# Optimization experiments

Hardware: AMD Instinct MI355X
Metric: run time of the kernel (lower is better)

## Reference

```python
import jax, jax.numpy as jnp
import numpy as np

V, E, H = 32000, 256, 512   # vocab, embed_dim, hidden_dim
B, S, T = 16, 512, 128      # batch, src_len, tgt_len
PAD = 0
H2 = 2 * H                  # decoder hidden size


def setup_inputs() -> dict:
    key = jax.random.key(0)
    ks = jax.random.split(key, 20)
    g = lambda k, shape: jax.random.normal(k, shape, dtype=jnp.float32) * 0.05
    emb = g(ks[0], (V, E)).at[PAD].set(0.0)  # padding_idx row zeroed
    inp = {
        "src": jax.random.randint(ks[18], (B, S), 0, V, dtype=jnp.int32),
        "tgt": jax.random.randint(ks[19], (B, T), 0, V, dtype=jnp.int32),
        "emb": emb,
        # encoder forward direction (torch gate order i,f,g,o)
        "Wih_f": g(ks[1], (4 * H, E)), "Whh_f": g(ks[2], (4 * H, H)),
        "bih_f": g(ks[3], (4 * H,)),   "bhh_f": g(ks[4], (4 * H,)),
        # encoder backward direction
        "Wih_b": g(ks[5], (4 * H, E)), "Whh_b": g(ks[6], (4 * H, H)),
        "bih_b": g(ks[7], (4 * H,)),   "bhh_b": g(ks[8], (4 * H,)),
        # decoder LSTM: input E+2H, hidden 2H
        "Wih_d": g(ks[9], (4 * H2, E + H2)), "Whh_d": g(ks[10], (4 * H2, H2)),
        "bih_d": g(ks[11], (4 * H2,)),       "bhh_d": g(ks[12], (4 * H2,)),
        # attention Linear(4H -> 2H)
        "Wa": g(ks[13], (H2, 2 * H2)), "ba": g(ks[14], (H2,)),
        # output Linear(2H -> V)
        "Wo": g(ks[15], (V, H2)), "bo": g(ks[16], (V,)),
    }
    return inp


def _lstm_cell(x, h, c, Wih, Whh, bih, bhh):
    z = x @ Wih.T + h @ Whh.T + bih + bhh
    i, f, g, o = jnp.split(z, 4, axis=-1)
    c = jax.nn.sigmoid(f) * c + jax.nn.sigmoid(i) * jnp.tanh(g)
    h = jax.nn.sigmoid(o) * jnp.tanh(c)
    return h, c


def _lstm_scan(xs, h0, c0, Wih, Whh, bih, bhh):
    def step(carry, x):
        h, c = _lstm_cell(x, carry[0], carry[1], Wih, Whh, bih, bhh)
        return (h, c), h
    (hT, cT), hs = jax.lax.scan(step, (h0, c0), xs)
    return hs, hT, cT


def reference(src, tgt, emb, Wih_f, Whh_f, bih_f, bhh_f, Wih_b, Whh_b, bih_b, bhh_b,
              Wih_d, Whh_d, bih_d, bhh_d, Wa, ba, Wo, bo):
    z = jnp.zeros((B, H), dtype=emb.dtype)
    xs = emb[src].transpose(1, 0, 2)                       # [S,B,E]
    hs_f, hTf, _ = _lstm_scan(xs,        z, z, Wih_f, Whh_f, bih_f, bhh_f)
    hs_b, hTb, _ = _lstm_scan(xs[::-1],  z, z, Wih_b, Whh_b, bih_b, bhh_b)
    enc_out = jnp.concatenate([hs_f, hs_b[::-1]], -1).transpose(1, 0, 2)  # [B,S,2H]
    h = jnp.concatenate([hTf, hTb], -1)                    # decoder h0 [B,2H]
    c = jnp.zeros_like(h)  # note: original reuses encoder c_n; see combined c0 below
    # original uses c_n (last cells) as decoder c0:
    _, _, cTf = _lstm_scan(xs, z, z, Wih_f, Whh_f, bih_f, bhh_f)[1], None, None
    # recompute cleanly (scan already returned cT above; redo properly):
    hs_f2, hTf2, cTf2 = _lstm_scan(xs,       z, z, Wih_f, Whh_f, bih_f, bhh_f)
    hs_b2, hTb2, cTb2 = _lstm_scan(xs[::-1], z, z, Wih_b, Whh_b, bih_b, bhh_b)
    c = jnp.concatenate([cTf2, cTb2], -1)

    Wa_h, Wa_e = Wa[:, :H2], Wa[:, H2:]
    enc_proj = jnp.einsum('bsd,kd->bsk', enc_out, Wa_e) + ba  # [B,S,2H]

    dec_xs = emb[tgt[:, :T - 1]].transpose(1, 0, 2)        # [T-1,B,E] teacher-forced

    def dec_step(carry, x):
        h, c = carry
        energy = jnp.tanh(enc_proj + (h @ Wa_h.T)[:, None, :])  # [B,S,2H]
        w = jax.nn.softmax(energy.sum(-1), axis=1)              # [B,S]
        ctx = jnp.einsum('bs,bsd->bd', w, enc_out)              # [B,2H]
        xi = jnp.concatenate([x, ctx], -1)                      # [B,E+2H]
        h, c = _lstm_cell(xi, h, c, Wih_d, Whh_d, bih_d, bhh_d)
        pred = h @ Wo.T + bo                                    # [B,V]
        return (h, c), pred

    _, preds = jax.lax.scan(dec_step, (h, c), dec_xs)           # [T-1,B,V]
    outputs = jnp.concatenate(
        [jnp.zeros((B, 1, V), dtype=preds.dtype), preds.transpose(1, 0, 2)], axis=1)
    return outputs
```

## Files before the change

### kernel.cpp

```cpp
#include <hip/hip_runtime.h>

typedef unsigned int uint;
typedef unsigned short ushort;
typedef unsigned long long ull;
typedef __attribute__((ext_vector_type(8))) short bf16x8;
typedef __attribute__((ext_vector_type(4))) float f32x4;

static constexpr int V_ = 32000, E_ = 256, H_ = 512, B_ = 16, S_ = 512, T_ = 128;
static constexpr int H2_ = 1024, G4_ = 2048, D4_ = 4096, KXI_ = 2304;
static constexpr int DSTEPS = T_ - 1;
static constexpr int MD = 2048;
static constexpr int NWG_DEC = 256;
static constexpr float LOG2E = 1.4426950408889634f;
static constexpr int ASTR = 2312;

#define DEVFN __device__ __forceinline__

DEVFN ushort f2bf(float f){ uint u = __builtin_bit_cast(uint, f); u += 0x7fffu + ((u>>16)&1u); return (ushort)(u>>16); }
DEVFN float bf2f(ushort h){ uint u = ((uint)h)<<16; return __builtin_bit_cast(float, u); }
DEVFN float fsig(float x){ float e = __builtin_amdgcn_exp2f(-LOG2E*x); return __builtin_amdgcn_rcpf(1.f+e); }
DEVFN float ftanh(float x){ x = fminf(15.f,fmaxf(-15.f,x)); float e = __builtin_amdgcn_exp2f(2.f*LOG2E*x); return (e-1.f)*__builtin_amdgcn_rcpf(e+1.f); }
DEVFN f32x4 mfma16(bf16x8 a, bf16x8 b, f32x4 c){ return __builtin_amdgcn_mfma_f32_16x16x32_bf16(a,b,c,0,0,0); }

struct ull2v{ ull x, y; };
DEVFN ull ald64(const void* p){ return __hip_atomic_load((const ull*)p, __ATOMIC_RELAXED, __HIP_MEMORY_SCOPE_AGENT); }
DEVFN uint ald32u(const uint* p){ return __hip_atomic_load(p, __ATOMIC_RELAXED, __HIP_MEMORY_SCOPE_AGENT); }
DEVFN float ald_f32(const float* p){ uint v = __hip_atomic_load((const uint*)p, __ATOMIC_RELAXED, __HIP_MEMORY_SCOPE_AGENT); return __builtin_bit_cast(float, v); }
DEVFN void ast32(float* p, float v){ __hip_atomic_store(p, v, __ATOMIC_RELAXED, __HIP_MEMORY_SCOPE_AGENT); }
DEVFN void ast16(ushort* p, ushort v){ __hip_atomic_store(p, v, __ATOMIC_RELAXED, __HIP_MEMORY_SCOPE_AGENT); }
DEVFN void astu(uint* p, uint v){ __hip_atomic_store(p, v, __ATOMIC_RELAXED, __HIP_MEMORY_SCOPE_AGENT); }

DEVFN void lbar(uint* lflags, int grp, int mem, int tid, uint& rnd){
  __syncthreads();
  rnd++;
  if (tid==0) astu(lflags + grp*16 + mem, rnd);
  if (tid<16){
    while (ald32u(lflags + grp*16 + tid) < rnd) __builtin_amdgcn_s_sleep(1);
  }
  __syncthreads();
}

__global__ void k_init(uint* __restrict__ flags, uint* __restrict__ hgf, uint* __restrict__ hgb,
                       uint* __restrict__ hU, uint* __restrict__ ctxU){
  int i = blockIdx.x*256 + threadIdx.x;
  if (i < 1024) flags[i] = 0;
  if (i < 2*B_*H_){ hgf[i]=0u; hgb[i]=0u; }
  if (i < B_*H2_) hU[i] = 0u;
  if (i < 2*B_*H2_) ctxU[i] = 0u;
}

__global__ void k_embed(const int* __restrict__ src, const int* __restrict__ tgt,
                        const float* __restrict__ emb, ushort* __restrict__ Xb, ushort* __restrict__ DXb){
  int r = blockIdx.x, tid = threadIdx.x;
  if (r < S_*B_){
    int s = r>>4, b = r&15;
    int id = src[b*S_+s];
    Xb[(size_t)r*E_+tid] = f2bf(emb[(size_t)id*E_+tid]);
  } else {
    int r2 = r - S_*B_;
    int t = r2>>4, b = r2&15;
    int id = tgt[b*T_+t];
    DXb[(size_t)r2*E_+tid] = f2bf(emb[(size_t)id*E_+tid]);
  }
}

__global__ void k_cvt_encw(const float* __restrict__ src, ushort* __restrict__ dst){
  int d = blockIdx.x;
  int wg = d>>7, r = d&127;
  int w = r>>4, jj=(r>>2)&3, g=r&3;
  int srow = g*H_ + wg*32 + w*4 + jj;
  for (int c = threadIdx.x; c < E_; c += 256)
    dst[(size_t)d*E_ + c] = f2bf(src[(size_t)srow*E_ + c]);
}

__global__ void k_bias_encp(const float* __restrict__ bih, const float* __restrict__ bhh, float* __restrict__ dst){
  int d = blockIdx.x*256 + threadIdx.x;
  int wg = d>>7, r = d&127;
  int w = r>>4, jj=(r>>2)&3, g=r&3;
  int srow = g*H_ + wg*32 + w*4 + jj;
  dst[d] = bih[srow]+bhh[srow];
}

__global__ void k_cvt_decw(const float* __restrict__ Wih_d, const float* __restrict__ Whh_d,
                           ushort* __restrict__ dst){
  int d = blockIdx.x;
  int wg = d>>4, r = d&15, jj = r>>2, g = r&3;
  int srow = g*H2_ + wg*4 + jj;
  for (int c = threadIdx.x; c < KXI_; c += 256){
    float v = (c < E_+H2_) ? Wih_d[(size_t)srow*(E_+H2_) + c] : Whh_d[(size_t)srow*H2_ + (c - (E_+H2_))];
    dst[(size_t)d*KXI_ + c] = f2bf(v);
  }
}

__global__ void k_bias_decp(const float* __restrict__ bih, const float* __restrict__ bhh, float* __restrict__ dst){
  int d = blockIdx.x*256 + threadIdx.x;
  int wg = d>>4, r = d&15, jj = r>>2, g = r&3;
  int srow = g*H2_ + wg*4 + jj;
  dst[d] = bih[srow]+bhh[srow];
}

__global__ void k_cvt_strided(const float* __restrict__ src, ushort* __restrict__ dst,
                              int cols, int sld, int soff, int dld, int doff){
  int r = blockIdx.x;
  for (int c = threadIdx.x; c < cols; c += 256)
    dst[(size_t)r*dld + doff + c] = f2bf(src[(size_t)r*sld + soff + c]);
}

__global__ void k_zero_t0(float* __restrict__ out){
  int i = blockIdx.x*256 + threadIdx.x;
  if (i < B_*V_){ int b = i / V_, v = i - b*V_; out[(size_t)b*T_*V_ + v] = 0.f; }
}

template<int MODE>
__global__ __launch_bounds__(256) void gemm128(const ushort* __restrict__ A, const ushort* __restrict__ Bm,
    const float* __restrict__ bias, void* __restrict__ outp, int M, int N, int K, int Mvalid){
  __shared__ __align__(16) ushort As[128*32];
  __shared__ __align__(16) ushort Bs[128*32];
  int tid = threadIdx.x;
  int wave = tid>>6, lane = tid&63;
  int m0 = blockIdx.y*128, n0 = blockIdx.x*128;
  int wm = wave>>1, wn = wave&1;
  int col = lane&15, rg = lane>>4;
  f32x4 acc[4][4];
  #pragma unroll
  for (int i=0;i<4;i++)
    #pragma unroll
    for (int j=0;j<4;j++) acc[i][j] = {0.f,0.f,0.f,0.f};
  for (int k0=0;k0<K;k0+=32){
    __syncthreads();
    #pragma unroll
    for (int j=0;j<2;j++){
      int li = j*256+tid;
      int row = li>>2, ko = (li&3)*8;
      *(bf16x8*)(As + li*8) = *(const bf16x8*)(A + (size_t)(m0+row)*K + k0 + ko);
      *(bf16x8*)(Bs + li*8) = *(const bf16x8*)(Bm + (size_t)(n0+row)*K + k0 + ko);
    }
    __syncthreads();
    bf16x8 af[4], bfr[4];
    #pragma unroll
    for (int f=0;f<4;f++){
      af[f]  = *(const bf16x8*)(As + (wm*64+f*16+col)*32 + rg*8);
      bfr[f] = *(const bf16x8*)(Bs + (wn*64+f*16+col)*32 + rg*8);
    }
    #pragma unroll
    for (int fm=0;fm<4;fm++)
      #pragma unroll
      for (int fn=0;fn<4;fn++)
        acc[fm][fn] = mfma16(af[fm], bfr[fn], acc[fm][fn]);
  }
  #pragma unroll
  for (int fm=0;fm<4;fm++){
    int mrow = m0 + wm*64 + fm*16 + rg*4;
    #pragma unroll
    for (int fn=0;fn<4;fn++){
      int gcol = n0 + wn*64 + fn*16 + col;
      float bv = bias ? bias[gcol] : 0.f;
      #pragma unroll
      for (int i=0;i<4;i++){
        float v = acc[fm][fn][i] + bv;
        int grow = mrow + i;
        if (MODE==0) ((float*)outp)[(size_t)grow*N + gcol] = v;
        else if (MODE==1) ((ushort*)outp)[(size_t)grow*N + gcol] = f2bf(v);
        else if (MODE==3) ((ushort*)outp)[(size_t)(grow>>4)*(16*2048) + gcol*16 + (grow&15)] = f2bf(v);
        else { if (grow < Mvalid){ int b = grow&15, t = grow>>4;
               ((float*)outp)[(size_t)b*T_*V_ + (size_t)(t+1)*V_ + gcol] = v; } }
      }
    }
  }
}

__global__ __launch_bounds__(512) void k_enc_persist(
    const ushort* __restrict__ Xgf, const ushort* __restrict__ Xgb,
    const float* __restrict__ Whhf, const float* __restrict__ Whhb,
    ushort* __restrict__ enc, ushort* __restrict__ enct,
    uint* __restrict__ hbuf1, float* __restrict__ cbuf0,
    uint* __restrict__ hgf, uint* __restrict__ hgb){
  const int dir = blockIdx.x >> 4;
  const int wg  = blockIdx.x & 15;
  const ushort* Xg = dir ? Xgb : Xgf;
  const float* Whh = dir ? Whhb : Whhf;
  uint* hg = dir ? hgb : hgf;
  __shared__ __align__(16) ushort Wlds[128*512];
  __shared__ __align__(16) ushort hls[16*512];
  int tid = threadIdx.x;
  for (int it=0; it<32; ++it){
    int r = it*4 + (tid>>7), ct = tid&127;
    int w_ = r>>4, jj=(r>>2)&3, g=r&3;
    int srow = g*H_ + wg*32 + w_*4 + jj;
    float4 v = *(const float4*)(Whh + (size_t)srow*H_ + ct*4);
    ushort4 o; o.x=f2bf(v.x); o.y=f2bf(v.y); o.z=f2bf(v.z); o.w=f2bf(v.w);
    int byte = (r*1024 + ct*8) ^ ((r&7)<<4);
    *(ushort4*)((char*)Wlds + byte) = o;
  }
  int w = tid>>6, lane = tid&63, colL = lane&15, rg = lane>>4;
  int gg = colL&3;
  float cst[4];
  #pragma unroll
  for (int i=0;i<4;i++) cst[i]=0.f;
  __syncthreads();
  for (int t=0;t<S_;++t){
    int pos = dir ? (S_-1-t) : t;
    const uint* hsrcU = hg + (t&1)*B_*H_;
    int colg = wg*128 + w*16 + colL;
    ushort4 xv = *(const ushort4*)(Xg + ((size_t)pos*2048 + colg)*16 + rg*4);
    uint uu[16];
    for(;;){
      #pragma unroll
      for (int k2=0;k2<2;k2++){
        int idx = tid + k2*512;
        const uint* p = hsrcU + (idx>>6)*H_ + (idx&63)*8;
        #pragma unroll
        for (int j=0;j<4;j++){
          ull v = ald64(p + j*2);
          uu[k2*8+j*2] = (uint)v; uu[k2*8+j*2+1] = (uint)(v>>32);
        }
      }
      bool ok = true;
      #pragma unroll
      for (int i2=0;i2<16;i2++) ok &= ((uu[i2]>>16) == (uint)t);
      if (ok) break;
      __builtin_amdgcn_s_sleep(1);
    }
    f32x4 acc;
    acc[0]=bf2f(xv.x); acc[1]=bf2f(xv.y); acc[2]=bf2f(xv.z); acc[3]=bf2f(xv.w);
    #pragma unroll
    for (int k2=0;k2<2;k2++){
      int idx = tid + k2*512;
      int byte = ((idx>>6)*1024 + (idx&63)*16) ^ (((idx>>6)&7)<<4);
      ushort tmp[8];
      #pragma unroll
      for (int j=0;j<8;j++) tmp[j] = (ushort)uu[k2*8+j];
      *(bf16x8*)((char*)hls + byte) = *(bf16x8*)tmp;
    }
    __syncthreads();
    int rowb = w*16 + colL;
    int base = rowb*1024 + rg*16, xm = (rowb&7)<<4;
    int hbase = colL*1024 + rg*16, hxm = (colL&7)<<4;
    #pragma unroll
    for (int kt=0;kt<16;kt++){
      bf16x8 afv = *(const bf16x8*)((const char*)hls + ((hbase + kt*64) ^ hxm));
      bf16x8 bfv = *(const bf16x8*)((const char*)Wlds + ((base + kt*64) ^ xm));
      acc = mfma16(afv, bfv, acc);
    }
    uint* hdstU = hg + ((t+1)&1)*B_*H_;
    #pragma unroll
    for (int i=0;i<4;i++){
      float v0 = acc[i];
      float v1 = __shfl_xor(v0, 1);
      float v2 = __shfl_xor(v0, 2);
      float v3 = __shfl_xor(v1, 2);
      float zi = gg==0?v0: gg==1?v1: gg==2?v2: v3;
      float zf = (gg^1)==0?v0: (gg^1)==1?v1: (gg^1)==2?v2: v3;
      float zg = (gg^2)==0?v0: (gg^2)==1?v1: (gg^2)==2?v2: v3;
      float zo = (gg^3)==0?v0: (gg^3)==1?v1: (gg^3)==2?v2: v3;
      float cc = fsig(zf)*cst[i] + fsig(zi)*ftanh(zg);
      cst[i] = cc;
      float h = fsig(zo)*ftanh(cc);
      if (gg==0){
        int j = wg*32 + w*4 + (colL>>2);
        int b = rg*4+i;
        ushort hb = f2bf(h);
        enc[((size_t)b*S_ + pos)*H2_ + dir*H_ + j] = hb;
        enct[((size_t)b*H2_ + dir*H_ + j)*S_ + pos] = hb;
        astu(&hdstU[b*H_ + j], (uint)hb | ((uint)(t+1)<<16));
        if (t==S_-1){
          hbuf1[b*H2_ + dir*H_ + j] = (uint)hb;
          cbuf0[b*H2_ + dir*H_ + j] = cc;
        }
      }
    }
    __syncthreads();
  }
}

__global__ __launch_bounds__(512) void k_dec(
    const float* __restrict__ P, const ushort* __restrict__ WaH,
    const ushort* __restrict__ Wd, const float* __restrict__ bsd,
    const ushort* __restrict__ enct, const ushort* __restrict__ DXb,
    const float* __restrict__ cbuf0, uint* __restrict__ hU,
    uint* __restrict__ ctxU, float* __restrict__ qbuf,
    float* __restrict__ scores, ushort* __restrict__ hsd,
    uint* __restrict__ flags){
  __shared__ __align__(16) ushort AB[16*ASTR];
  __shared__ __align__(16) float pr[8*256];
  __shared__ float redz[256];
  __shared__ float qls[1024];
  __shared__ float wls[512];
  __shared__ float part[512];
  __shared__ float red[16];
  __shared__ float cst[64];
  uint* lflags = flags + 256;
  uint* qf     = flags + 768;
  int wgid = blockIdx.x, tid = threadIdx.x;
  int w = tid>>6, lane = tid&63, colL = lane&15, rg = lane>>4;
  int b = wgid>>4, wc = wgid&15;
  uint rnd = 0;
  if (tid < 64){
    int jj = tid>>4, b4 = tid&15;
    cst[tid] = cbuf0[b4*H2_ + wgid*4 + jj];
  }
  for (int st=0; st<DSTEPS; ++st){
    const uint* hprevU = hU + ((st+1)&1)*B_*H2_;
    uint* cslot = ctxU + (st&1)*B_*H2_;
    const uint wantH = (uint)st;
    const uint wantC = (uint)(st+1);
    float* qslot = qbuf + (st&1)*B_*H2_;
    if (wgid >= 64 && wgid < 128){
      int n0 = (wgid-64)*16;
      const ushort* Bp = WaH + (size_t)(n0+colL)*H2_ + w*128 + rg*8;
      bf16x8 bwa[4];
      #pragma unroll
      for (int kt=0;kt<4;kt++) bwa[kt] = *(const bf16x8*)(Bp + kt*32);
      const uint* hp = hprevU + colL*H2_ + w*128 + rg*8;
      uint uu[32];
      for(;;){
        #pragma unroll
        for (int kt=0;kt<4;kt++)
          #pragma unroll
          for (int j=0;j<4;j++){
            ull v = ald64(hp + kt*32 + j*2);
            uu[kt*8+j*2] = (uint)v; uu[kt*8+j*2+1] = (uint)(v>>32);
          }
        bool ok = true;
        #pragma unroll
        for (int i2=0;i2<32;i2++) ok &= ((uu[i2]>>16) == wantH);
        if (ok) break;
        __builtin_amdgcn_s_sleep(1);
      }
      f32x4 acc = {0.f,0.f,0.f,0.f};
      #pragma unroll
      for (int kt=0;kt<4;kt++){
        ushort tmp[8];
        #pragma unroll
        for (int j=0;j<8;j++) tmp[j] = (ushort)uu[kt*8+j];
        acc = mfma16(*(bf16x8*)tmp, bwa[kt], acc);
      }
      *(f32x4*)&pr[w*256 + lane*4] = acc;
      __syncthreads();
      if (tid < 256){
        float s = pr[tid];
        #pragma unroll
        for (int w8=1;w8<8;w8++) s += pr[w8*256 + tid];
        int l = tid>>2, i = tid&3;
        ast32(&qslot[(size_t)((l>>4)*4 + i)*H2_ + n0 + (l&15)], s);
      }
      __syncthreads();
      if (tid==0) astu(qf + (wgid-64), wantC);
    }
    f32x4 pv[16];
    {
      int rbase = b*S_ + wc*32 + w*4;
      #pragma unroll
      for (int rr=0;rr<4;rr++){
        const f32x4* Pr = (const f32x4*)(P + (size_t)(rbase+rr)*H2_) + lane*4;
        #pragma unroll
        for (int u=0;u<4;u++) pv[rr*4+u] = Pr[u];
      }
    }
    if (tid < 64){
      while (ald32u(qf + tid) < wantC) __builtin_amdgcn_s_sleep(1);
    }
    __syncthreads();
    {
      ull q2 = ald64((const ull*)(qslot + (size_t)b*H2_) + tid);
      *(ull*)&qls[tid*2] = q2;
      __syncthreads();
      f32x4 qv[4];
      #pragma unroll
      for (int u=0;u<4;u++) qv[u] = *(const f32x4*)&qls[lane*16 + u*4];
      int rbase = b*S_ + wc*32 + w*4;
      #pragma unroll
      for (int rr=0;rr<4;rr++){
        float s = 0.f;
        #pragma unroll
        for (int u=0;u<4;u++){
          f32x4 p4 = pv[rr*4+u];
          s += ftanh(p4[0]+qv[u][0])+ftanh(p4[1]+qv[u][1])+ftanh(p4[2]+qv[u][2])+ftanh(p4[3]+qv[u][3]);
        }
        #pragma unroll
        for (int o=32;o;o>>=1) s += __shfl_xor(s,o);
        if (lane==0) ast32(&scores[rbase+rr], s);
      }
    }
    bf16x8 ev[8];
    {
      int c = wc*64 + (tid&63), sseg = tid>>6;
      const ushort* ep = enct + ((size_t)b*H2_ + c)*S_ + sseg*64;
      #pragma unroll
      for (int u=0;u<8;u++) ev[u] = *(const bf16x8*)(ep + u*8);
    }
    lbar(lflags, b, wc, tid, rnd);
    {
      float sc = ald_f32(scores + b*S_ + tid);
      float m = sc;
      #pragma unroll
      for (int o=32;o;o>>=1) m = fmaxf(m, __shfl_xor(m,o));
      if (lane==0) red[w] = m;
      __syncthreads();
      m = red[0];
      #pragma unroll
      for (int k2=1;k2<8;k2++) m = fmaxf(m, red[k2]);
      float e = __builtin_amdgcn_exp2f((sc - m)*LOG2E);
      float ss = e;
      #pragma unroll
      for (int o=32;o;o>>=1) ss += __shfl_xor(ss,o);
      if (lane==0) red[8+w] = ss;
      __syncthreads();
      float tot = red[8];
      #pragma unroll
      for (int k2=9;k2<16;k2++) tot += red[k2];
      wls[tid] = e * __builtin_amdgcn_rcpf(tot);
      __syncthreads();
      int sseg = tid>>6;
      float a = 0.f;
      #pragma unroll
      for (int u=0;u<8;u++){
        #pragma unroll
        for (int j=0;j<8;j++) a += wls[sseg*64 + u*8 + j] * bf2f((ushort)ev[u][j]);
      }
      part[tid] = a;
      __syncthreads();
      if (tid < 64){
        float s = part[tid];
        #pragma unroll
        for (int g2=1;g2<8;g2++) s += part[g2*64 + tid];
        astu(&cslot[b*H2_ + wc*64 + tid], (uint)f2bf(s) | (wantC<<16));
      }
    }
    {
      { int b3 = tid>>5, seg = tid&31;
        *(bf16x8*)&AB[b3*ASTR + seg*8] = *(const bf16x8*)(DXb + (size_t)(st*16+b3)*E_ + seg*8); }
      bf16x8 bw[9];
      {
        int row0 = wgid*16;
        const ushort* Bp = Wd + (size_t)(row0+colL)*KXI_ + w*288 + rg*8;
        #pragma unroll
        for (int kt=0;kt<9;kt++) bw[kt] = *(const bf16x8*)(Bp + kt*32);
      }
      uint uc[32], uh[32];
      for(;;){
        #pragma unroll
        for (int k2=0;k2<4;k2++){
          int idx = tid + k2*512;
          const uint* pc = cslot  + (idx>>7)*H2_ + (idx&127)*8;
          const uint* ph = hprevU + (idx>>7)*H2_ + (idx&127)*8;
          #pragma unroll
          for (int j=0;j<4;j++){
            ull vc = ald64(pc + j*2);
            ull vh = ald64(ph + j*2);
            uc[k2*8+j*2] = (uint)vc; uc[k2*8+j*2+1] = (uint)(vc>>32);
            uh[k2*8+j*2] = (uint)vh; uh[k2*8+j*2+1] = (uint)(vh>>32);
          }
        }
        bool ok = true;
        #pragma unroll
        for (int i2=0;i2<32;i2++) ok &= ((uc[i2]>>16) == wantC) && ((uh[i2]>>16) == wantH);
        if (ok) break;
        __builtin_amdgcn_s_sleep(1);
      }
      #pragma unroll
      for (int k2=0;k2<4;k2++){
        int idx = tid + k2*512;
        ushort tc[8], th[8];
        #pragma unroll
        for (int j=0;j<8;j++){ tc[j] = (ushort)uc[k2*8+j]; th[j] = (ushort)uh[k2*8+j]; }
        *(bf16x8*)&AB[(idx>>7)*ASTR + 256  + (idx&127)*8] = *(bf16x8*)tc;
        *(bf16x8*)&AB[(idx>>7)*ASTR + 1280 + (idx&127)*8] = *(bf16x8*)th;
      }
      __syncthreads();
      int row0 = wgid*16;
      f32x4 acc = {0.f,0.f,0.f,0.f};
      const ushort* Apb = &AB[colL*ASTR + w*288 + rg*8];
      #pragma unroll
      for (int kt=0;kt<9;kt++)
        acc = mfma16(*(const bf16x8*)(Apb + kt*32), bw[kt], acc);
      *(f32x4*)&pr[w*256 + lane*4] = acc;
      __syncthreads();
      if (tid < 256){
        float s = bsd[row0 + ((tid>>2)&15)];
        #pragma unroll
        for (int w8=0;w8<8;w8++) s += pr[w8*256 + tid];
        redz[tid] = s;
      }
      __syncthreads();
      if (tid < 64){
        int jj = tid>>4, b4 = tid&15, rgc = b4>>2, ic = b4&3;
        float zi = redz[((jj*4+0) + 16*rgc)*4 + ic];
        float zf = redz[((jj*4+1) + 16*rgc)*4 + ic];
        float zg = redz[((jj*4+2) + 16*rgc)*4 + ic];
        float zo = redz[((jj*4+3) + 16*rgc)*4 + ic];
        float cc2 = fsig(zf)*cst[tid] + fsig(zi)*ftanh(zg);
        cst[tid] = cc2;
        float h = fsig(zo)*ftanh(cc2);
        ushort hb = f2bf(h);
        int j = wgid*4 + jj;
        astu(&hU[(st&1)*B_*H2_ + b4*H2_ + j], (uint)hb | ((uint)(st+1)<<16));
        hsd[((size_t)st*B_ + b4)*H2_ + j] = hb;
      }
      __syncthreads();
    }
  }
}

extern "C" void kernel_launch(void* const* d_in, const int* in_sizes, int n_in,
                              void* d_out, int out_size, void* d_ws, size_t ws_size,
                              hipStream_t stream) {
  const int* src   = (const int*)d_in[0];
  const int* tgt   = (const int*)d_in[1];
  const float* emb   = (const float*)d_in[2];
  const float* Wih_f = (const float*)d_in[3];
  const float* Whh_f = (const float*)d_in[4];
  const float* bih_f = (const float*)d_in[5];
  const float* bhh_f = (const float*)d_in[6];
  const float* Wih_b = (const float*)d_in[7];
  const float* Whh_b = (const float*)d_in[8];
  const float* bih_b = (const float*)d_in[9];
  const float* bhh_b = (const float*)d_in[10];
  const float* Wih_d = (const float*)d_in[11];
  const float* Whh_d = (const float*)d_in[12];
  const float* bih_d = (const float*)d_in[13];
  const float* bhh_d = (const float*)d_in[14];
  const float* Wa    = (const float*)d_in[15];
  const float* ba    = (const float*)d_in[16];
  const float* Wo    = (const float*)d_in[17];
  const float* bo    = (const float*)d_in[18];
  float* out = (float*)d_out;
  (void)in_sizes; (void)n_in; (void)out_size; (void)ws_size;

  char* ws = (char*)d_ws;
  size_t off = 0;
  auto alloc = [&](size_t bytes)->char*{ char* p = ws + off; off += (bytes + 255) & ~(size_t)255; return p; };
  ushort* Xb     = (ushort*)alloc((size_t)S_*B_*E_*2);
  ushort* DXb    = (ushort*)alloc((size_t)DSTEPS*B_*E_*2);
  ushort* Wihf_p = (ushort*)alloc((size_t)G4_*E_*2);
  ushort* Wihb_p = (ushort*)alloc((size_t)G4_*E_*2);
  float*  bsf    = (float*)alloc(G4_*4);
  float*  bsb    = (float*)alloc(G4_*4);
  ushort* ENC    = (ushort*)alloc((size_t)B_*S_*H2_*2);
  ushort* ENCT   = (ushort*)alloc((size_t)B_*S_*H2_*2);
  ushort* WaH    = (ushort*)alloc((size_t)H2_*H2_*2);
  ushort* WaE    = (ushort*)alloc((size_t)H2_*H2_*2);
  ushort* Wd     = (ushort*)alloc((size_t)D4_*KXI_*2);
  float*  bsd    = (float*)alloc(D4_*4);
  ushort* WoB    = (ushort*)alloc((size_t)V_*H2_*2);
  float*  cbuf0  = (float*)alloc(B_*H2_*4);
  uint*   hU     = (uint*)alloc((size_t)2*B_*H2_*4);
  uint*   ctxU   = (uint*)alloc((size_t)2*B_*H2_*4);
  float*  qbuf   = (float*)alloc((size_t)2*B_*H2_*4);
  float*  scores = (float*)alloc(B_*S_*4);
  ushort* hsd    = (ushort*)alloc((size_t)MD*H2_*2);
  uint*   hgf    = (uint*)alloc((size_t)2*B_*H_*4);
  uint*   hgb    = (uint*)alloc((size_t)2*B_*H_*4);
  uint*   flags  = (uint*)alloc(4096);
  char*   big    = alloc((size_t)2*S_*B_*G4_*2);
  ushort* Xgf = (ushort*)big;
  ushort* Xgb = (ushort*)(big + (size_t)S_*B_*G4_*2);
  float*  P   = (float*)big;

  k_init<<<dim3(128), dim3(256), 0, stream>>>(flags, hgf, hgb, hU, ctxU);
  k_embed<<<dim3(S_*B_ + DSTEPS*B_), dim3(E_), 0, stream>>>(src, tgt, emb, Xb, DXb);
  k_cvt_encw<<<dim3(G4_), dim3(256), 0, stream>>>(Wih_f, Wihf_p);
  k_cvt_encw<<<dim3(G4_), dim3(256), 0, stream>>>(Wih_b, Wihb_p);
  k_bias_encp<<<dim3(8), dim3(256), 0, stream>>>(bih_f, bhh_f, bsf);
  k_bias_encp<<<dim3(8), dim3(256), 0, stream>>>(bih_b, bhh_b, bsb);
  k_cvt_strided<<<dim3(H2_), dim3(256), 0, stream>>>(Wa, WaH, H2_, 2*H2_, 0,   H2_, 0);
  k_cvt_strided<<<dim3(H2_), dim3(256), 0, stream>>>(Wa, WaE, H2_, 2*H2_, H2_, H2_, 0);
  k_cvt_decw<<<dim3(D4_), dim3(256), 0, stream>>>(Wih_d, Whh_d, Wd);
  k_bias_decp<<<dim3(16), dim3(256), 0, stream>>>(bih_d, bhh_d, bsd);
  k_cvt_strided<<<dim3(V_),  dim3(256), 0, stream>>>(Wo, WoB, H2_, H2_, 0, H2_, 0);

  gemm128<3><<<dim3(G4_/128, (S_*B_)/128), dim3(256), 0, stream>>>(Xb, Wihf_p, bsf, Xgf, S_*B_, G4_, E_, 0);
  gemm128<3><<<dim3(G4_/128, (S_*B_)/128), dim3(256), 0, stream>>>(Xb, Wihb_p, bsb, Xgb, S_*B_, G4_, E_, 0);

  k_enc_persist<<<dim3(32), dim3(512), 0, stream>>>(Xgf, Xgb, Whh_f, Whh_b, ENC, ENCT,
                                                    hU + B_*H2_, cbuf0, hgf, hgb);

  gemm128<0><<<dim3(H2_/128, (B_*S_)/128), dim3(256), 0, stream>>>(ENC, WaE, ba, P, B_*S_, H2_, H2_, 0);
  k_zero_t0<<<dim3((B_*V_+255)/256), dim3(256), 0, stream>>>(out);

  k_dec<<<dim3(NWG_DEC), dim3(512), 0, stream>>>(P, WaH, Wd, bsd, ENCT, DXb, cbuf0, hU,
                                                 ctxU, qbuf, scores, hsd, flags);

  gemm128<2><<<dim3(V_/128, MD/128), dim3(256), 0, stream>>>(hsd, WoB, bo, out, MD, V_, H2_, DSTEPS*B_);
}
```

Before: 5.856 ms.

## Replace decoder flag barriers with step-tagged data words for q and scores

The decoder's separate flag arrays and local group barrier for the attention query and score exchange are removed. Each fp32 value is now stored as a 64-bit word holding a hi/lo bf16 split plus a step tag, and consumers poll the data directly until the tag matches. This drops a round of flag stores, polling and barrier latency on every decoder step. In exchange, operand prefetches (WaH, Wd, enct, P rows, Xg) that used to be issued before the waits now happen after them, and each value costs more traffic and pack/unpack work.

```diff
diff --git a/kernel.cpp b/kernel.cpp
--- a/kernel.cpp
+++ b/kernel.cpp
@@ -29,24 +29,27 @@
 DEVFN void ast32(float* p, float v){ __hip_atomic_store(p, v, __ATOMIC_RELAXED, __HIP_MEMORY_SCOPE_AGENT); }
 DEVFN void ast16(ushort* p, ushort v){ __hip_atomic_store(p, v, __ATOMIC_RELAXED, __HIP_MEMORY_SCOPE_AGENT); }
 DEVFN void astu(uint* p, uint v){ __hip_atomic_store(p, v, __ATOMIC_RELAXED, __HIP_MEMORY_SCOPE_AGENT); }
-
-DEVFN void lbar(uint* lflags, int grp, int mem, int tid, uint& rnd){
-  __syncthreads();
-  rnd++;
-  if (tid==0) astu(lflags + grp*16 + mem, rnd);
-  if (tid<16){
-    while (ald32u(lflags + grp*16 + tid) < rnd) __builtin_amdgcn_s_sleep(1);
-  }
-  __syncthreads();
-}
+DEVFN void ast64(ull* p, ull v){ __hip_atomic_store(p, v, __ATOMIC_RELAXED, __HIP_MEMORY_SCOPE_AGENT); }
+
+DEVFN float unpack2f(ull v){ return bf2f((ushort)v) + bf2f((ushort)(v>>32)); }
+DEVFN ull pack2f(float s, uint tag){
+  ushort hi = f2bf(s);
+  float r = s - bf2f(hi);
+  ushort lo = f2bf(r);
+  return ((ull)((tag<<16)|(uint)lo)<<32) | (ull)((tag<<16)|(uint)hi);
+}
+DEVFN bool tagok2(ull v, uint tag){ return ((((uint)v)>>16)==tag) && ((((uint)(v>>32))>>16)==tag); }
 
 __global__ void k_init(uint* __restrict__ flags, uint* __restrict__ hgf, uint* __restrict__ hgb,
-                       uint* __restrict__ hU, uint* __restrict__ ctxU){
+                       uint* __restrict__ hU, uint* __restrict__ ctxU,
+                       uint* __restrict__ qUu, uint* __restrict__ sUu){
   int i = blockIdx.x*256 + threadIdx.x;
   if (i < 1024) flags[i] = 0;
   if (i < 2*B_*H_){ hgf[i]=0u; hgb[i]=0u; }
   if (i < B_*H2_) hU[i] = 0u;
   if (i < 2*B_*H2_) ctxU[i] = 0u;
+  if (i < 2*B_*H2_) qUu[i] = 0u;
+  if (i < B_*S_)  { sUu[i*2] = 0u; sUu[i*2+1] = 0u; }
 }
 
 __global__ void k_embed(const int* __restrict__ src, const int* __restrict__ tgt,
@@ -201,8 +204,6 @@
   for (int t=0;t<S_;++t){
     int pos = dir ? (S_-1-t) : t;
     const uint* hsrcU = hg + (t&1)*B_*H_;
-    int colg = wg*128 + w*16 + colL;
-    ushort4 xv = *(const ushort4*)(Xg + ((size_t)pos*2048 + colg)*16 + rg*4);
     uint uu[16];
     for(;;){
       #pragma unroll
@@ -221,6 +222,8 @@
       if (ok) break;
       __builtin_amdgcn_s_sleep(1);
     }
+    int colg = wg*128 + w*16 + colL;
+    ushort4 xv = *(const ushort4*)(Xg + ((size_t)pos*2048 + colg)*16 + rg*4);
     f32x4 acc;
     acc[0]=bf2f(xv.x); acc[1]=bf2f(xv.y); acc[2]=bf2f(xv.z); acc[3]=bf2f(xv.w);
     #pragma unroll
@@ -278,9 +281,8 @@
     const ushort* __restrict__ Wd, const float* __restrict__ bsd,
     const ushort* __restrict__ enct, const ushort* __restrict__ DXb,
     const float* __restrict__ cbuf0, uint* __restrict__ hU,
-    uint* __restrict__ ctxU, float* __restrict__ qbuf,
-    float* __restrict__ scores, ushort* __restrict__ hsd,
-    uint* __restrict__ flags){
+    uint* __restrict__ ctxU, ull* __restrict__ qU,
+    ull* __restrict__ sU, ushort* __restrict__ hsd){
   __shared__ __align__(16) ushort AB[16*ASTR];
   __shared__ __align__(16) float pr[8*256];
   __shared__ float redz[256];
@@ -289,12 +291,9 @@
   __shared__ float part[512];
   __shared__ float red[16];
   __shared__ float cst[64];
-  uint* lflags = flags + 256;
-  uint* qf     = flags + 768;
   int wgid = blockIdx.x, tid = threadIdx.x;
   int w = tid>>6, lane = tid&63, colL = lane&15, rg = lane>>4;
   int b = wgid>>4, wc = wgid&15;
-  uint rnd = 0;
   if (tid < 64){
     int jj = tid>>4, b4 = tid&15;
     cst[tid] = cbuf0[b4*H2_ + wgid*4 + jj];
@@ -303,14 +302,9 @@
     const uint* hprevU = hU + ((st+1)&1)*B_*H2_;
     uint* cslot = ctxU + (st&1)*B_*H2_;
     const uint wantH = (uint)st;
-    const uint wantC = (uint)(st+1);
-    float* qslot = qbuf + (st&1)*B_*H2_;
+    const uint wantT = (uint)(st+1);
     if (wgid >= 64 && wgid < 128){
       int n0 = (wgid-64)*16;
-      const ushort* Bp = WaH + (size_t)(n0+colL)*H2_ + w*128 + rg*8;
-      bf16x8 bwa[4];
-      #pragma unroll
-      for (int kt=0;kt<4;kt++) bwa[kt] = *(const bf16x8*)(Bp + kt*32);
       const uint* hp = hprevU + colL*H2_ + w*128 + rg*8;
       uint uu[32];
       for(;;){
@@ -328,12 +322,13 @@
         __builtin_amdgcn_s_sleep(1);
       }
       f32x4 acc = {0.f,0.f,0.f,0.f};
+      const ushort* Bp = WaH + (size_t)(n0+colL)*H2_ + w*128 + rg*8;
       #pragma unroll
       for (int kt=0;kt<4;kt++){
         ushort tmp[8];
         #pragma unroll
         for (int j=0;j<8;j++) tmp[j] = (ushort)uu[kt*8+j];
-        acc = mfma16(*(bf16x8*)tmp, bwa[kt], acc);
+        acc = mfma16(*(bf16x8*)tmp, *(const bf16x8*)(Bp + kt*32), acc);
       }
       *(f32x4*)&pr[w*256 + lane*4] = acc;
       __syncthreads();
@@ -342,56 +337,50 @@
         #pragma unroll
         for (int w8=1;w8<8;w8++) s += pr[w8*256 + tid];
         int l = tid>>2, i = tid&3;
-        ast32(&qslot[(size_t)((l>>4)*4 + i)*H2_ + n0 + (l&15)], s);
-      }
-      __syncthreads();
-      if (tid==0) astu(qf + (wgid-64), wantC);
-    }
-    f32x4 pv[16];
+        ast64(&qU[(size_t)((l>>4)*4 + i)*H2_ + n0 + (l&15)], pack2f(s, wantT));
+      }
+    }
     {
+      const ull* qp = qU + (size_t)b*H2_;
+      ull v0, v1;
+      for(;;){
+        v0 = ald64(qp + tid*2);
+        v1 = ald64(qp + tid*2 + 1);
+        if (tagok2(v0, wantT) && tagok2(v1, wantT)) break;
+        __builtin_amdgcn_s_sleep(1);
+      }
+      qls[tid*2]   = unpack2f(v0);
+      qls[tid*2+1] = unpack2f(v1);
+      __syncthreads();
+      f32x4 qv[4];
+      #pragma unroll
+      for (int u=0;u<4;u++) qv[u] = *(const f32x4*)&qls[lane*16 + u*4];
       int rbase = b*S_ + wc*32 + w*4;
       #pragma unroll
       for (int rr=0;rr<4;rr++){
-        const f32x4* Pr = (const f32x4*)(P + (size_t)(rbase+rr)*H2_) + lane*4;
-        #pragma unroll
-        for (int u=0;u<4;u++) pv[rr*4+u] = Pr[u];
-      }
-    }
-    if (tid < 64){
-      while (ald32u(qf + tid) < wantC) __builtin_amdgcn_s_sleep(1);
+        int r = rbase + rr;
+        const float4* Pr = (const float4*)(P + (size_t)r*H2_) + lane*4;
+        float s = 0.f;
+        #pragma unroll
+        for (int u=0;u<4;u++){
+          float4 pv = Pr[u];
+          s += ftanh(pv.x+qv[u][0])+ftanh(pv.y+qv[u][1])+ftanh(pv.z+qv[u][2])+ftanh(pv.w+qv[u][3]);
+        }
+        #pragma unroll
+        for (int o=32;o;o>>=1) s += __shfl_xor(s,o);
+        if (lane==0) ast64(&sU[r], pack2f(s, wantT));
+      }
     }
     __syncthreads();
     {
-      ull q2 = ald64((const ull*)(qslot + (size_t)b*H2_) + tid);
-      *(ull*)&qls[tid*2] = q2;
-      __syncthreads();
-      f32x4 qv[4];
-      #pragma unroll
-      for (int u=0;u<4;u++) qv[u] = *(const f32x4*)&qls[lane*16 + u*4];
-      int rbase = b*S_ + wc*32 + w*4;
-      #pragma unroll
-      for (int rr=0;rr<4;rr++){
-        float s = 0.f;
-        #pragma unroll
-        for (int u=0;u<4;u++){
-          f32x4 p4 = pv[rr*4+u];
-          s += ftanh(p4[0]+qv[u][0])+ftanh(p4[1]+qv[u][1])+ftanh(p4[2]+qv[u][2])+ftanh(p4[3]+qv[u][3]);
-        }
-        #pragma unroll
-        for (int o=32;o;o>>=1) s += __shfl_xor(s,o);
-        if (lane==0) ast32(&scores[rbase+rr], s);
-      }
-    }
-    bf16x8 ev[8];
-    {
-      int c = wc*64 + (tid&63), sseg = tid>>6;
-      const ushort* ep = enct + ((size_t)b*H2_ + c)*S_ + sseg*64;
-      #pragma unroll
-      for (int u=0;u<8;u++) ev[u] = *(const bf16x8*)(ep + u*8);
-    }
-    lbar(lflags, b, wc, tid, rnd);
-    {
-      float sc = ald_f32(scores + b*S_ + tid);
+      ull sv;
+      const ull* sp = sU + (size_t)b*S_ + tid;
+      for(;;){
+        sv = ald64(sp);
+        if (tagok2(sv, wantT)) break;
+        __builtin_amdgcn_s_sleep(1);
+      }
+      float sc = unpack2f(sv);
       float m = sc;
       #pragma unroll
       for (int o=32;o;o>>=1) m = fmaxf(m, __shfl_xor(m,o));
@@ -411,12 +400,14 @@
       for (int k2=9;k2<16;k2++) tot += red[k2];
       wls[tid] = e * __builtin_amdgcn_rcpf(tot);
       __syncthreads();
-      int sseg = tid>>6;
+      int c = wc*64 + (tid&63), sseg = tid>>6;
+      const ushort* ep = enct + ((size_t)b*H2_ + c)*S_ + sseg*64;
       float a = 0.f;
       #pragma unroll
       for (int u=0;u<8;u++){
-        #pragma unroll
-        for (int j=0;j<8;j++) a += wls[sseg*64 + u*8 + j] * bf2f((ushort)ev[u][j]);
+        bf16x8 ev = *(const bf16x8*)(ep + u*8);
+        #pragma unroll
+        for (int j=0;j<8;j++) a += wls[sseg*64 + u*8 + j] * bf2f((ushort)ev[j]);
       }
       part[tid] = a;
       __syncthreads();
@@ -424,19 +415,12 @@
         float s = part[tid];
         #pragma unroll
         for (int g2=1;g2<8;g2++) s += part[g2*64 + tid];
-        astu(&cslot[b*H2_ + wc*64 + tid], (uint)f2bf(s) | (wantC<<16));
+        astu(&cslot[b*H2_ + wc*64 + tid], (uint)f2bf(s) | (wantT<<16));
       }
     }
     {
       { int b3 = tid>>5, seg = tid&31;
         *(bf16x8*)&AB[b3*ASTR + seg*8] = *(const bf16x8*)(DXb + (size_t)(st*16+b3)*E_ + seg*8); }
-      bf16x8 bw[9];
-      {
-        int row0 = wgid*16;
-        const ushort* Bp = Wd + (size_t)(row0+colL)*KXI_ + w*288 + rg*8;
-        #pragma unroll
-        for (int kt=0;kt<9;kt++) bw[kt] = *(const bf16x8*)(Bp + kt*32);
-      }
       uint uc[32], uh[32];
       for(;;){
         #pragma unroll
@@ -454,7 +438,7 @@
         }
         bool ok = true;
         #pragma unroll
-        for (int i2=0;i2<32;i2++) ok &= ((uc[i2]>>16) == wantC) && ((uh[i2]>>16) == wantH);
+        for (int i2=0;i2<32;i2++) ok &= ((uc[i2]>>16) == wantT) && ((uh[i2]>>16) == wantH);
         if (ok) break;
         __builtin_amdgcn_s_sleep(1);
       }
@@ -470,10 +454,11 @@
       __syncthreads();
       int row0 = wgid*16;
       f32x4 acc = {0.f,0.f,0.f,0.f};
+      const ushort* Bp = Wd + (size_t)(row0+colL)*KXI_ + w*288 + rg*8;
       const ushort* Apb = &AB[colL*ASTR + w*288 + rg*8];
       #pragma unroll
       for (int kt=0;kt<9;kt++)
-        acc = mfma16(*(const bf16x8*)(Apb + kt*32), bw[kt], acc);
+        acc = mfma16(*(const bf16x8*)(Apb + kt*32), *(const bf16x8*)(Bp + kt*32), acc);
       *(f32x4*)&pr[w*256 + lane*4] = acc;
       __syncthreads();
       if (tid < 256){
@@ -494,7 +479,7 @@
         float h = fsig(zo)*ftanh(cc2);
         ushort hb = f2bf(h);
         int j = wgid*4 + jj;
-        astu(&hU[(st&1)*B_*H2_ + b4*H2_ + j], (uint)hb | ((uint)(st+1)<<16));
+        astu(&hU[(st&1)*B_*H2_ + b4*H2_ + j], (uint)hb | (wantT<<16));
         hsd[((size_t)st*B_ + b4)*H2_ + j] = hb;
       }
       __syncthreads();
@@ -546,8 +531,8 @@
   float*  cbuf0  = (float*)alloc(B_*H2_*4);
   uint*   hU     = (uint*)alloc((size_t)2*B_*H2_*4);
   uint*   ctxU   = (uint*)alloc((size_t)2*B_*H2_*4);
-  float*  qbuf   = (float*)alloc((size_t)2*B_*H2_*4);
-  float*  scores = (float*)alloc(B_*S_*4);
+  ull*    qU     = (ull*)alloc((size_t)B_*H2_*8);
+  ull*    sU     = (ull*)alloc((size_t)B_*S_*8);
   ushort* hsd    = (ushort*)alloc((size_t)MD*H2_*2);
   uint*   hgf    = (uint*)alloc((size_t)2*B_*H_*4);
   uint*   hgb    = (uint*)alloc((size_t)2*B_*H_*4);
@@ -557,7 +542,7 @@
   ushort* Xgb = (ushort*)(big + (size_t)S_*B_*G4_*2);
   float*  P   = (float*)big;
 
-  k_init<<<dim3(128), dim3(256), 0, stream>>>(flags, hgf, hgb, hU, ctxU);
+  k_init<<<dim3(128), dim3(256), 0, stream>>>(flags, hgf, hgb, hU, ctxU, (uint*)qU, (uint*)sU);
   k_embed<<<dim3(S_*B_ + DSTEPS*B_), dim3(E_), 0, stream>>>(src, tgt, emb, Xb, DXb);
   k_cvt_encw<<<dim3(G4_), dim3(256), 0, stream>>>(Wih_f, Wihf_p);
   k_cvt_encw<<<dim3(G4_), dim3(256), 0, stream>>>(Wih_b, Wihb_p);
@@ -579,7 +564,7 @@
   k_zero_t0<<<dim3((B_*V_+255)/256), dim3(256), 0, stream>>>(out);
 
   k_dec<<<dim3(NWG_DEC), dim3(512), 0, stream>>>(P, WaH, Wd, bsd, ENCT, DXb, cbuf0, hU,
-                                                 ctxU, qbuf, scores, hsd, flags);
+                                                 ctxU, qU, sU, hsd);
 
   gemm128<2><<<dim3(V_/128, MD/128), dim3(256), 0, stream>>>(hsd, WoB, bo, out, MD, V_, H2_, DSTEPS*B_);
 }
```

Measured after the change: 5.574 ms. -4.8%, faster.
